# Optimization experiments

Measured on AMD Instinct MI355X. Metric: run time of the kernel, lower is better.

## Reference

```python
import jax, jax.numpy as jnp
import numpy as np

BATCH = 1024
D = 256          # input_size == embed_size (forced by elementwise multiply)
NUM_REL = 42     # num_classes + 2
FEAT = 30


def setup_inputs() -> dict:
    key = jax.random.key(0)
    k_x, k_q, k_f, k_r = jax.random.split(key, 4)
    x = jax.random.normal(k_x, (BATCH, D), dtype=jnp.float32)
    x_mask = jnp.ones((BATCH,), dtype=bool)  # unused by the module body
    q = jax.random.randint(k_q, (BATCH, BATCH), 0, NUM_REL, dtype=jnp.int64)
    f = jax.random.normal(k_f, (BATCH, FEAT), dtype=jnp.float32)  # unused by the module body
    # relation embedding table, init std=0.001, row 0 zeroed (padding relation)
    R_emb = jax.random.normal(k_r, (NUM_REL, D), dtype=jnp.float32) * 0.001
    R_emb = R_emb.at[0].set(0.0)
    return {"x": x, "x_mask": x_mask, "q": q, "f": f, "R_emb": R_emb}


def reference(x, x_mask, q, f, R_emb):
    # r[i,j,d] = R_emb[q[i,j], d]   (the big O(B^2*D) gather)
    r = R_emb[q]  # [B, B, D]
    # attn[i,j] = sum_d r[i,j,d] * x[j,d] * x[i,d]
    attn = jnp.einsum('ijd,jd,id->ij', r, x, x)  # [B, B]
    weights = jax.nn.softmax(attn, axis=-1)
    outputs = weights @ x  # [B, D]
    return outputs
```

## Files before the change

### kernel.cpp

```cpp
#include <hip/hip_runtime.h>
#include <hip/hip_bf16.h>

#define BB 1024
#define DD 256
#define NREL 42
#define AST 264

typedef __attribute__((ext_vector_type(8))) short short8_t;
typedef __attribute__((ext_vector_type(4))) short short4_t;
typedef __attribute__((ext_vector_type(4))) float f32x4;
typedef __attribute__((ext_vector_type(4))) int   i32x4;
typedef __attribute__((ext_vector_type(4))) unsigned int u32x4;

__device__ __forceinline__ unsigned short bf16_of(float f) {
    unsigned u = __float_as_uint(f);
    return (unsigned short)((u + 0x7FFFu + ((u >> 16) & 1u)) >> 16);
}

__device__ __forceinline__ float blo(unsigned u) { return __uint_as_float(u << 16); }
__device__ __forceinline__ float bhi(unsigned u) { return __uint_as_float(u & 0xFFFF0000u); }

__device__ __forceinline__ float dot8bf(u32x4 av, u32x4 xv, float acc) {
    acc = fmaf(blo(av[0]), blo(xv[0]), acc);
    acc = fmaf(bhi(av[0]), bhi(xv[0]), acc);
    acc = fmaf(blo(av[1]), blo(xv[1]), acc);
    acc = fmaf(bhi(av[1]), bhi(xv[1]), acc);
    acc = fmaf(blo(av[2]), blo(xv[2]), acc);
    acc = fmaf(bhi(av[2]), bhi(xv[2]), acc);
    acc = fmaf(blo(av[3]), blo(xv[3]), acc);
    acc = fmaf(bhi(av[3]), bhi(xv[3]), acc);
    return acc;
}

__global__ __launch_bounds__(256) void cvt_kernel(const float* __restrict__ x,
                                                  unsigned short* __restrict__ xh8,
                                                  unsigned short* __restrict__ xbfT) {
    __shared__ float t32[64][68];
    const int bj = blockIdx.x * 64;
    const int bd = blockIdx.y * 64;
    const int tid = threadIdx.x;
    const int tr = tid >> 4;
    const int tc = tid & 15;

    #pragma unroll
    for (int rr = 0; rr < 4; ++rr) {
        const int jl = rr * 16 + tr;
        const f32x4 v = *reinterpret_cast<const f32x4*>(&x[(bj + jl) * DD + bd + tc * 4]);
        *reinterpret_cast<f32x4*>(&t32[jl][tc * 4]) = v;
    }
    __syncthreads();

    #pragma unroll
    for (int rr = 0; rr < 4; ++rr) {
        const int dl = rr * 16 + tr;
        short4_t h;
        #pragma unroll
        for (int e = 0; e < 4; ++e) h[e] = (short)bf16_of(t32[tc * 4 + e][dl]);
        *reinterpret_cast<short4_t*>(&xbfT[(bd + dl) * BB + bj + tc * 4]) = h;
    }

    #pragma unroll
    for (int c = 0; c < 2; ++c) {
        const int idx = c * 256 + tid;
        const int jl  = idx & 63;
        const int d8l = idx >> 6;
        short8_t hv;
        #pragma unroll
        for (int e = 0; e < 8; ++e) hv[e] = (short)bf16_of(t32[jl][d8l * 8 + e]);
        *reinterpret_cast<short8_t*>(
            &xh8[(size_t)((bd >> 3) + d8l) * (BB * 8) + (bj + jl) * 8]) = hv;
    }
}

__global__ __launch_bounds__(256) void attn_kernel(const float* __restrict__ x,
                                                   const int* __restrict__ q,
                                                   const float* __restrict__ R,
                                                   const unsigned short* __restrict__ xh8,
                                                   unsigned short* __restrict__ P) {
    __shared__ __align__(16) unsigned short Ah[NREL * AST];
    __shared__ float s_attn[BB];
    __shared__ unsigned short s_qs[BB];

    const int tid  = threadIdx.x;
    const int w    = tid >> 6;
    const int lane = tid & 63;
    const int i    = blockIdx.x;

    {
        const int c4 = tid * 4;
        const i32x4 qa = *reinterpret_cast<const i32x4*>(&q[i * BB + c4]);
        short4_t sa;
        sa[0] = (short)qa[0]; sa[1] = (short)qa[1];
        sa[2] = (short)qa[2]; sa[3] = (short)qa[3];
        *reinterpret_cast<short4_t*>(&s_qs[c4]) = sa;
    }

    for (int c = tid; c < NREL * 32; c += 256) {
        const int k  = c >> 5;
        const int d0 = (c & 31) * 8;
        const f32x4 r0 = *reinterpret_cast<const f32x4*>(&R[k * DD + d0]);
        const f32x4 r1 = *reinterpret_cast<const f32x4*>(&R[k * DD + d0 + 4]);
        const f32x4 x0 = *reinterpret_cast<const f32x4*>(&x[i * DD + d0]);
        const f32x4 x1 = *reinterpret_cast<const f32x4*>(&x[i * DD + d0 + 4]);
        short8_t hv;
        #pragma unroll
        for (int e = 0; e < 4; ++e) {
            hv[e]     = (short)bf16_of(r0[e] * x0[e]);
            hv[e + 4] = (short)bf16_of(r1[e] * x1[e]);
        }
        *reinterpret_cast<short8_t*>(&Ah[k * AST + d0]) = hv;
    }

    __syncthreads();

    const int j0 = w * 256 + lane;
    const unsigned short* a0 = &Ah[(int)s_qs[j0]       * AST];
    const unsigned short* a1 = &Ah[(int)s_qs[j0 + 64]  * AST];
    const unsigned short* a2 = &Ah[(int)s_qs[j0 + 128] * AST];
    const unsigned short* a3 = &Ah[(int)s_qs[j0 + 192] * AST];
    const unsigned short* xp = xh8 + (size_t)j0 * 8;

    float acc0 = 0.f, acc1 = 0.f, acc2 = 0.f, acc3 = 0.f;

    #pragma unroll 2
    for (int d8 = 0; d8 < 32; ++d8) {
        const unsigned short* xb = xp + (size_t)d8 * (BB * 8);
        const u32x4 xv0 = *reinterpret_cast<const u32x4*>(xb);
        const u32x4 xv1 = *reinterpret_cast<const u32x4*>(xb + 64 * 8);
        const u32x4 xv2 = *reinterpret_cast<const u32x4*>(xb + 128 * 8);
        const u32x4 xv3 = *reinterpret_cast<const u32x4*>(xb + 192 * 8);

        const int ao = d8 * 8;
        const u32x4 av0 = *reinterpret_cast<const u32x4*>(a0 + ao);
        const u32x4 av1 = *reinterpret_cast<const u32x4*>(a1 + ao);
        const u32x4 av2 = *reinterpret_cast<const u32x4*>(a2 + ao);
        const u32x4 av3 = *reinterpret_cast<const u32x4*>(a3 + ao);

        acc0 = dot8bf(av0, xv0, acc0);
        acc1 = dot8bf(av1, xv1, acc1);
        acc2 = dot8bf(av2, xv2, acc2);
        acc3 = dot8bf(av3, xv3, acc3);
    }

    s_attn[j0]       = acc0;
    s_attn[j0 + 64]  = acc1;
    s_attn[j0 + 128] = acc2;
    s_attn[j0 + 192] = acc3;

    __syncthreads();

    f32x4 v4[4];
    #pragma unroll
    for (int kk = 0; kk < 4; ++kk)
        v4[kk] = *reinterpret_cast<const f32x4*>(&s_attn[kk * 256 + lane * 4]);

    float m = -1e30f;
    #pragma unroll
    for (int kk = 0; kk < 4; ++kk)
        m = fmaxf(m, fmaxf(fmaxf(v4[kk][0], v4[kk][1]), fmaxf(v4[kk][2], v4[kk][3])));
    #pragma unroll
    for (int off = 1; off < 64; off <<= 1) m = fmaxf(m, __shfl_xor(m, off));

    float e[16];
    float ssum = 0.f;
    #pragma unroll
    for (int kk = 0; kk < 4; ++kk)
        #pragma unroll
        for (int ee = 0; ee < 4; ++ee) {
            const float t2 = __expf(v4[kk][ee] - m);
            e[kk * 4 + ee] = t2;
            ssum += t2;
        }
    #pragma unroll
    for (int off = 1; off < 64; off <<= 1) ssum += __shfl_xor(ssum, off);
    const float inv = 1.0f / ssum;

    {
        short4_t pv;
        #pragma unroll
        for (int ee = 0; ee < 4; ++ee) pv[ee] = (short)bf16_of(e[w * 4 + ee] * inv);
        *reinterpret_cast<short4_t*>(&P[i * BB + w * 256 + lane * 4]) = pv;
    }
}

__global__ __launch_bounds__(256) void out_partial(const unsigned short* __restrict__ P,
                                                   const unsigned short* __restrict__ xbfT,
                                                   float* __restrict__ part) {
    const int tid = threadIdx.x;
    const int wave = tid >> 6, lane = tid & 63;
    const int lcol = lane & 15;
    const int lk8  = (lane >> 4) * 8;
    const int i0 = blockIdx.y * 64 + wave * 16;
    const int d0 = blockIdx.x * 64;
    const int k0 = blockIdx.z * 256;

    f32x4 acc[4];
    #pragma unroll
    for (int nt = 0; nt < 4; ++nt) acc[nt] = (f32x4)0.0f;

    #pragma unroll
    for (int ks = 0; ks < 8; ++ks) {
        const short8_t a = *reinterpret_cast<const short8_t*>(
            &P[(i0 + lcol) * BB + k0 + ks * 32 + lk8]);
        #pragma unroll
        for (int nt = 0; nt < 4; ++nt) {
            const short8_t b = *reinterpret_cast<const short8_t*>(
                &xbfT[(d0 + nt * 16 + lcol) * BB + k0 + ks * 32 + lk8]);
            acc[nt] = __builtin_amdgcn_mfma_f32_16x16x32_bf16(a, b, acc[nt], 0, 0, 0);
        }
    }

    const int rbase = (lane >> 4) * 4;
    float* pz = part + (size_t)blockIdx.z * BB * DD;
    #pragma unroll
    for (int r = 0; r < 4; ++r)
        #pragma unroll
        for (int nt = 0; nt < 4; ++nt)
            pz[(i0 + rbase + r) * DD + d0 + nt * 16 + lcol] = acc[nt][r];
}

__global__ __launch_bounds__(256) void out_reduce(const float* __restrict__ part,
                                                  float* __restrict__ out) {
    const int idx = blockIdx.x * DD + threadIdx.x;
    out[idx] = (part[idx] + part[BB * DD + idx]) +
               (part[2 * BB * DD + idx] + part[3 * BB * DD + idx]);
}

extern "C" void kernel_launch(void* const* d_in, const int* in_sizes, int n_in,
                              void* d_out, int out_size, void* d_ws, size_t ws_size,
                              hipStream_t stream) {
    (void)in_sizes; (void)n_in; (void)out_size; (void)ws_size;
    const float* x = (const float*)d_in[0];
    const int* q = (const int*)d_in[2];
    const float* R = (const float*)d_in[4];
    float* out = (float*)d_out;

    char* ws = (char*)d_ws;
    unsigned short* xh8  = (unsigned short*)(ws);
    unsigned short* xbfT = (unsigned short*)(ws + (512u << 10));
    unsigned short* P    = (unsigned short*)(ws + (1024u << 10));
    float*          part = (float*)(ws + (3072u << 10));

    cvt_kernel<<<dim3(16, 4), 256, 0, stream>>>(x, xh8, xbfT);
    attn_kernel<<<dim3(BB), 256, 0, stream>>>(x, q, R, xh8, P);
    out_partial<<<dim3(4, 16, 4), 256, 0, stream>>>(P, xbfT, part);
    out_reduce<<<dim3(BB), 256, 0, stream>>>(part, out);
}
```

Before: 48.82 us.

## Process two query rows per attention block to reuse x loads

Each attn_kernel block now handles two rows i instead of one and keeps two bf16 A tables in shared memory. Every x vector loaded from global memory feeds both rows' dot products, which halves global x traffic per output. Softmax work is split across waves by row. The cost is double the shared memory, more registers, half as many blocks, and duplicated table-building work per block.

```diff
diff --git a/kernel.cpp b/kernel.cpp
--- a/kernel.cpp
+++ b/kernel.cpp
@@ -20,16 +20,17 @@
 __device__ __forceinline__ float blo(unsigned u) { return __uint_as_float(u << 16); }
 __device__ __forceinline__ float bhi(unsigned u) { return __uint_as_float(u & 0xFFFF0000u); }
 
-__device__ __forceinline__ float dot8bf(u32x4 av, u32x4 xv, float acc) {
-    acc = fmaf(blo(av[0]), blo(xv[0]), acc);
-    acc = fmaf(bhi(av[0]), bhi(xv[0]), acc);
-    acc = fmaf(blo(av[1]), blo(xv[1]), acc);
-    acc = fmaf(bhi(av[1]), bhi(xv[1]), acc);
-    acc = fmaf(blo(av[2]), blo(xv[2]), acc);
-    acc = fmaf(bhi(av[2]), bhi(xv[2]), acc);
-    acc = fmaf(blo(av[3]), blo(xv[3]), acc);
-    acc = fmaf(bhi(av[3]), bhi(xv[3]), acc);
-    return acc;
+__device__ __forceinline__ void dot8bf2(u32x4 aa, u32x4 ab, u32x4 xv,
+                                        float& ra, float& rb) {
+    #pragma unroll
+    for (int e = 0; e < 4; ++e) {
+        const float xl = blo(xv[e]);
+        const float xh = bhi(xv[e]);
+        ra = fmaf(blo(aa[e]), xl, ra);
+        ra = fmaf(bhi(aa[e]), xh, ra);
+        rb = fmaf(blo(ab[e]), xl, rb);
+        rb = fmaf(bhi(ab[e]), xh, rb);
+    }
 }
 
 __global__ __launch_bounds__(256) void cvt_kernel(const float* __restrict__ x,
@@ -77,50 +78,63 @@
                                                    const float* __restrict__ R,
                                                    const unsigned short* __restrict__ xh8,
                                                    unsigned short* __restrict__ P) {
-    __shared__ __align__(16) unsigned short Ah[NREL * AST];
-    __shared__ float s_attn[BB];
-    __shared__ unsigned short s_qs[BB];
+    __shared__ __align__(16) unsigned short Ah[2][NREL * AST];
+    __shared__ float s_attn[2][BB];
+    __shared__ unsigned short s_qs[2][BB];
 
     const int tid  = threadIdx.x;
     const int w    = tid >> 6;
     const int lane = tid & 63;
-    const int i    = blockIdx.x;
+    const int i0   = blockIdx.x * 2;
 
     {
-        const int c4 = tid * 4;
-        const i32x4 qa = *reinterpret_cast<const i32x4*>(&q[i * BB + c4]);
-        short4_t sa;
-        sa[0] = (short)qa[0]; sa[1] = (short)qa[1];
-        sa[2] = (short)qa[2]; sa[3] = (short)qa[3];
-        *reinterpret_cast<short4_t*>(&s_qs[c4]) = sa;
-    }
-
-    for (int c = tid; c < NREL * 32; c += 256) {
-        const int k  = c >> 5;
-        const int d0 = (c & 31) * 8;
-        const f32x4 r0 = *reinterpret_cast<const f32x4*>(&R[k * DD + d0]);
-        const f32x4 r1 = *reinterpret_cast<const f32x4*>(&R[k * DD + d0 + 4]);
-        const f32x4 x0 = *reinterpret_cast<const f32x4*>(&x[i * DD + d0]);
-        const f32x4 x1 = *reinterpret_cast<const f32x4*>(&x[i * DD + d0 + 4]);
-        short8_t hv;
-        #pragma unroll
-        for (int e = 0; e < 4; ++e) {
-            hv[e]     = (short)bf16_of(r0[e] * x0[e]);
-            hv[e + 4] = (short)bf16_of(r1[e] * x1[e]);
+        const int r  = tid >> 7;
+        const int c8 = (tid & 127) * 8;
+        const int qi = i0 + r;
+        const i32x4 qa = *reinterpret_cast<const i32x4*>(&q[qi * BB + c8]);
+        const i32x4 qb = *reinterpret_cast<const i32x4*>(&q[qi * BB + c8 + 4]);
+        short4_t sa, sb;
+        sa[0] = (short)qa[0]; sa[1] = (short)qa[1]; sa[2] = (short)qa[2]; sa[3] = (short)qa[3];
+        sb[0] = (short)qb[0]; sb[1] = (short)qb[1]; sb[2] = (short)qb[2]; sb[3] = (short)qb[3];
+        *reinterpret_cast<short4_t*>(&s_qs[r][c8])     = sa;
+        *reinterpret_cast<short4_t*>(&s_qs[r][c8 + 4]) = sb;
+    }
+
+    #pragma unroll
+    for (int i2 = 0; i2 < 2; ++i2) {
+        const int i = i0 + i2;
+        for (int c = tid; c < NREL * 32; c += 256) {
+            const int k  = c >> 5;
+            const int d0 = (c & 31) * 8;
+            const f32x4 r0 = *reinterpret_cast<const f32x4*>(&R[k * DD + d0]);
+            const f32x4 r1 = *reinterpret_cast<const f32x4*>(&R[k * DD + d0 + 4]);
+            const f32x4 x0 = *reinterpret_cast<const f32x4*>(&x[i * DD + d0]);
+            const f32x4 x1 = *reinterpret_cast<const f32x4*>(&x[i * DD + d0 + 4]);
+            short8_t hv;
+            #pragma unroll
+            for (int e = 0; e < 4; ++e) {
+                hv[e]     = (short)bf16_of(r0[e] * x0[e]);
+                hv[e + 4] = (short)bf16_of(r1[e] * x1[e]);
+            }
+            *reinterpret_cast<short8_t*>(&Ah[i2][k * AST + d0]) = hv;
         }
-        *reinterpret_cast<short8_t*>(&Ah[k * AST + d0]) = hv;
     }
 
     __syncthreads();
 
     const int j0 = w * 256 + lane;
-    const unsigned short* a0 = &Ah[(int)s_qs[j0]       * AST];
-    const unsigned short* a1 = &Ah[(int)s_qs[j0 + 64]  * AST];
-    const unsigned short* a2 = &Ah[(int)s_qs[j0 + 128] * AST];
-    const unsigned short* a3 = &Ah[(int)s_qs[j0 + 192] * AST];
+    const unsigned short* a00 = &Ah[0][(int)s_qs[0][j0]       * AST];
+    const unsigned short* a01 = &Ah[0][(int)s_qs[0][j0 + 64]  * AST];
+    const unsigned short* a02 = &Ah[0][(int)s_qs[0][j0 + 128] * AST];
+    const unsigned short* a03 = &Ah[0][(int)s_qs[0][j0 + 192] * AST];
+    const unsigned short* a10 = &Ah[1][(int)s_qs[1][j0]       * AST];
+    const unsigned short* a11 = &Ah[1][(int)s_qs[1][j0 + 64]  * AST];
+    const unsigned short* a12 = &Ah[1][(int)s_qs[1][j0 + 128] * AST];
+    const unsigned short* a13 = &Ah[1][(int)s_qs[1][j0 + 192] * AST];
     const unsigned short* xp = xh8 + (size_t)j0 * 8;
 
-    float acc0 = 0.f, acc1 = 0.f, acc2 = 0.f, acc3 = 0.f;
+    float c00 = 0.f, c01 = 0.f, c02 = 0.f, c03 = 0.f;
+    float c10 = 0.f, c11 = 0.f, c12 = 0.f, c13 = 0.f;
 
     #pragma unroll 2
     for (int d8 = 0; d8 < 32; ++d8) {
@@ -131,28 +145,36 @@
         const u32x4 xv3 = *reinterpret_cast<const u32x4*>(xb + 192 * 8);
 
         const int ao = d8 * 8;
-        const u32x4 av0 = *reinterpret_cast<const u32x4*>(a0 + ao);
-        const u32x4 av1 = *reinterpret_cast<const u32x4*>(a1 + ao);
-        const u32x4 av2 = *reinterpret_cast<const u32x4*>(a2 + ao);
-        const u32x4 av3 = *reinterpret_cast<const u32x4*>(a3 + ao);
-
-        acc0 = dot8bf(av0, xv0, acc0);
-        acc1 = dot8bf(av1, xv1, acc1);
-        acc2 = dot8bf(av2, xv2, acc2);
-        acc3 = dot8bf(av3, xv3, acc3);
-    }
-
-    s_attn[j0]       = acc0;
-    s_attn[j0 + 64]  = acc1;
-    s_attn[j0 + 128] = acc2;
-    s_attn[j0 + 192] = acc3;
+        const u32x4 av00 = *reinterpret_cast<const u32x4*>(a00 + ao);
+        const u32x4 av01 = *reinterpret_cast<const u32x4*>(a01 + ao);
+        const u32x4 av02 = *reinterpret_cast<const u32x4*>(a02 + ao);
+        const u32x4 av03 = *reinterpret_cast<const u32x4*>(a03 + ao);
+        const u32x4 av10 = *reinterpret_cast<const u32x4*>(a10 + ao);
+        const u32x4 av11 = *reinterpret_cast<const u32x4*>(a11 + ao);
+        const u32x4 av12 = *reinterpret_cast<const u32x4*>(a12 + ao);
+        const u32x4 av13 = *reinterpret_cast<const u32x4*>(a13 + ao);
+
+        dot8bf2(av00, av10, xv0, c00, c10);
+        dot8bf2(av01, av11, xv1, c01, c11);
+        dot8bf2(av02, av12, xv2, c02, c12);
+        dot8bf2(av03, av13, xv3, c03, c13);
+    }
+
+    s_attn[0][j0]       = c00;  s_attn[1][j0]       = c10;
+    s_attn[0][j0 + 64]  = c01;  s_attn[1][j0 + 64]  = c11;
+    s_attn[0][j0 + 128] = c02;  s_attn[1][j0 + 128] = c12;
+    s_attn[0][j0 + 192] = c03;  s_attn[1][j0 + 192] = c13;
 
     __syncthreads();
 
+    const int p2 = w & 1;
+    const int jh = w >> 1;
+    const int i  = i0 + p2;
+
     f32x4 v4[4];
     #pragma unroll
     for (int kk = 0; kk < 4; ++kk)
-        v4[kk] = *reinterpret_cast<const f32x4*>(&s_attn[kk * 256 + lane * 4]);
+        v4[kk] = *reinterpret_cast<const f32x4*>(&s_attn[p2][kk * 256 + lane * 4]);
 
     float m = -1e30f;
     #pragma unroll
@@ -175,11 +197,13 @@
     for (int off = 1; off < 64; off <<= 1) ssum += __shfl_xor(ssum, off);
     const float inv = 1.0f / ssum;
 
-    {
+    #pragma unroll
+    for (int kk2 = 0; kk2 < 2; ++kk2) {
+        const int kk = jh * 2 + kk2;
         short4_t pv;
         #pragma unroll
-        for (int ee = 0; ee < 4; ++ee) pv[ee] = (short)bf16_of(e[w * 4 + ee] * inv);
-        *reinterpret_cast<short4_t*>(&P[i * BB + w * 256 + lane * 4]) = pv;
+        for (int ee = 0; ee < 4; ++ee) pv[ee] = (short)bf16_of(e[kk * 4 + ee] * inv);
+        *reinterpret_cast<short4_t*>(&P[i * BB + kk * 256 + lane * 4]) = pv;
     }
 }
 
@@ -242,7 +266,7 @@
     float*          part = (float*)(ws + (3072u << 10));
 
     cvt_kernel<<<dim3(16, 4), 256, 0, stream>>>(x, xh8, xbfT);
-    attn_kernel<<<dim3(BB), 256, 0, stream>>>(x, q, R, xh8, P);
+    attn_kernel<<<dim3(512), 256, 0, stream>>>(x, q, R, xh8, P);
     out_partial<<<dim3(4, 16, 4), 256, 0, stream>>>(P, xbfT, part);
     out_reduce<<<dim3(BB), 256, 0, stream>>>(part, out);
 }
```

After: 43.79 us. -10.3%, faster.
